# Performance work log

Measured on AMD Instinct MI355X. Metric: run time of the kernel, lower is better.

## Reference

```python
import jax, jax.numpy as jnp
import numpy as np

SCALING = 32.0 / 8.0  # alpha / rank

def setup_inputs() -> dict:
    key = jax.random.key(0)
    k1, k2, k3, k4, k5 = jax.random.split(key, 5)
    B, S, D_in, D_out, R = 4, 2048, 1600, 4800, 8
    x = jax.random.normal(k1, (B, S, D_in), dtype=jnp.float32)
    W = jax.random.normal(k2, (D_in, D_out), dtype=jnp.float32) * 0.02
    b = jax.random.normal(k3, (D_out,), dtype=jnp.float32) * 0.02
    lora_A = jax.random.normal(k4, (D_in, R), dtype=jnp.float32) * 0.02
    lora_B = jax.random.normal(k5, (R, D_out), dtype=jnp.float32) * 0.02
    return {"x": x, "W": W, "b": b, "lora_A": lora_A, "lora_B": lora_B}

def reference(x, W, b, lora_A, lora_B):
    # base Conv1D: x @ W + b  (GPT-2 Conv1D semantics)
    base = jnp.einsum('bsd,df->bsf', x, W) + b
    # low-rank LoRA path: (x @ A) @ B, scaled
    lora = jnp.einsum('bsr,rf->bsf', jnp.einsum('bsd,dr->bsr', x, lora_A), lora_B)
    return base + lora * SCALING
```

## Files before the change

### kernel.cpp

```cpp
#include <hip/hip_runtime.h>
#include <hip/hip_bf16.h>


#define M_ROWS 8192
#define K_DIM  1600
#define N_DIM  4800
#define KP     1664

#define BM 128
#define BN 160
#define BK 64
#define KT (KP / BK)

typedef __attribute__((ext_vector_type(4))) float f32x4;
typedef __attribute__((ext_vector_type(8))) short s16x8;

static __device__ __forceinline__ unsigned short f2bf(float f) {
    unsigned int u = __float_as_uint(f);
    u += 0x7fffu + ((u >> 16) & 1u);
    return (unsigned short)(u >> 16);
}

typedef __attribute__((address_space(3))) unsigned int as3_uint;
typedef __attribute__((address_space(1))) const unsigned int as1_uint;

static __device__ __forceinline__ void gl16(const unsigned short* g,
                                            unsigned short* l) {
    __builtin_amdgcn_global_load_lds((as1_uint*)g, (as3_uint*)l, 16, 0, 0);
}

__global__ __launch_bounds__(256) void prep_x(const float* __restrict__ x,
                                              const float* __restrict__ lora_A,
                                              unsigned short* __restrict__ Xbp) {
    __shared__ float4 lA4[3200];
    const int t = threadIdx.x;
    for (int g = t; g < 3200; g += 256) lA4[g] = ((const float4*)lora_A)[g];
    __syncthreads();

    const int lane = t & 63;
    const int w    = t >> 6;

    for (int i = 0; i < 4; ++i) {
        const int m = blockIdx.x * 16 + w * 4 + i;
        const float* xrow = x + (size_t)m * K_DIM;
        unsigned short* orow = Xbp + (size_t)m * KP;

        float acc[8];
#pragma unroll
        for (int r = 0; r < 8; ++r) acc[r] = 0.f;

        for (int g = lane; g < 400; g += 64) {
            float4 xv = ((const float4*)xrow)[g];
            ushort4 o;
            o.x = f2bf(xv.x); o.y = f2bf(xv.y); o.z = f2bf(xv.z); o.w = f2bf(xv.w);
            ((ushort4*)orow)[g] = o;
            float xs[4] = {xv.x, xv.y, xv.z, xv.w};
#pragma unroll
            for (int j = 0; j < 4; ++j) {
                float4 l0 = lA4[(4 * g + j) * 2 + 0];
                float4 l1 = lA4[(4 * g + j) * 2 + 1];
                acc[0] += xs[j] * l0.x; acc[1] += xs[j] * l0.y;
                acc[2] += xs[j] * l0.z; acc[3] += xs[j] * l0.w;
                acc[4] += xs[j] * l1.x; acc[5] += xs[j] * l1.y;
                acc[6] += xs[j] * l1.z; acc[7] += xs[j] * l1.w;
            }
        }

#pragma unroll
        for (int off = 32; off > 0; off >>= 1)
#pragma unroll
            for (int r = 0; r < 8; ++r) acc[r] += __shfl_down(acc[r], off, 64);

        float xa[8];
#pragma unroll
        for (int r = 0; r < 8; ++r) xa[r] = __shfl(acc[r], 0, 64);

        if (lane < 16) {
            ushort4 o;
            if (lane == 0)      { o.x = f2bf(xa[0]); o.y = f2bf(xa[1]); o.z = f2bf(xa[2]); o.w = f2bf(xa[3]); }
            else if (lane == 1) { o.x = f2bf(xa[4]); o.y = f2bf(xa[5]); o.z = f2bf(xa[6]); o.w = f2bf(xa[7]); }
            else                { o.x = 0; o.y = 0; o.z = 0; o.w = 0; }
            ((ushort4*)orow)[400 + lane] = o;
        }
    }
}

__global__ __launch_bounds__(256) void prep_w(const float* __restrict__ W,
                                              unsigned short* __restrict__ Wtp) {
    __shared__ float tile[32][65];
    const int n0 = blockIdx.x * 64;
    const int k0 = blockIdx.y * 32;
    const int t  = threadIdx.x;

#pragma unroll
    for (int p = 0; p < 2; ++p) {
        const int k  = p * 16 + (t >> 4);
        const int c4 = (t & 15) * 4;
        float4 v = *(const float4*)(W + (size_t)(k0 + k) * N_DIM + n0 + c4);
        tile[k][c4 + 0] = v.x; tile[k][c4 + 1] = v.y;
        tile[k][c4 + 2] = v.z; tile[k][c4 + 3] = v.w;
    }
    __syncthreads();

    const int n   = t >> 2;
    const int seg = t & 3;
    unsigned int pk[4];
#pragma unroll
    for (int h = 0; h < 4; ++h) {
        unsigned int lo = f2bf(tile[seg * 8 + 2 * h + 0][n]);
        unsigned int hi = f2bf(tile[seg * 8 + 2 * h + 1][n]);
        pk[h] = lo | (hi << 16);
    }
    uint4 o = {pk[0], pk[1], pk[2], pk[3]};
    *(uint4*)(Wtp + (size_t)(n0 + n) * KP + k0 + seg * 8) = o;
}

__global__ __launch_bounds__(256) void prep_lb(const float* __restrict__ lora_B,
                                               unsigned short* __restrict__ Wtp) {
    const int n = blockIdx.x * 256 + threadIdx.x;
    if (n >= N_DIM) return;
    ushort4* d4 = (ushort4*)(Wtp + (size_t)n * KP + 1600);
    ushort4 o0, o1, z;
    o0.x = f2bf(4.0f * lora_B[0 * N_DIM + n]);
    o0.y = f2bf(4.0f * lora_B[1 * N_DIM + n]);
    o0.z = f2bf(4.0f * lora_B[2 * N_DIM + n]);
    o0.w = f2bf(4.0f * lora_B[3 * N_DIM + n]);
    o1.x = f2bf(4.0f * lora_B[4 * N_DIM + n]);
    o1.y = f2bf(4.0f * lora_B[5 * N_DIM + n]);
    o1.z = f2bf(4.0f * lora_B[6 * N_DIM + n]);
    o1.w = f2bf(4.0f * lora_B[7 * N_DIM + n]);
    z.x = 0; z.y = 0; z.z = 0; z.w = 0;
    d4[0] = o0;
    d4[1] = o1;
#pragma unroll
    for (int i = 2; i < 16; ++i) d4[i] = z;
}

__global__ __launch_bounds__(256, 3) void gemm_bt(const unsigned short* __restrict__ Ab,
                                                  const unsigned short* __restrict__ Bb,
                                                  const float* __restrict__ bias,
                                                  float* __restrict__ out) {
    __shared__ unsigned short lsA[BM * BK];
    __shared__ unsigned short lsB[BN * BK];

    const int t    = threadIdx.x;
    const int n0   = blockIdx.x * BN;
    const int m0   = blockIdx.y * BM;
    const int lane = t & 63;
    const int w    = t >> 6;
    const int wr   = (w >> 1) * 64;
    const int wc   = (w & 1) * 80;
    const int lr   = lane & 15;
    const int quad = lane >> 4;

    const int rS = lane >> 3;
    const int gS = ((lane & 7) ^ (rS & 7)) * 8;
    const unsigned short* srcA = Ab + (size_t)(m0 + rS) * KP + gS;
    const unsigned short* srcB = Bb + (size_t)(n0 + rS) * KP + gS;

    int rowA[4], rowB[5];
#pragma unroll
    for (int mt = 0; mt < 4; ++mt) rowA[mt] = (wr + mt * 16 + lr) * BK;
#pragma unroll
    for (int nt = 0; nt < 5; ++nt) rowB[nt] = (wc + nt * 16 + lr) * BK;
    const int lx = lr & 7;

    f32x4 acc[4][5];
#pragma unroll
    for (int mt = 0; mt < 4; ++mt)
#pragma unroll
        for (int nt = 0; nt < 5; ++nt) acc[mt][nt] = (f32x4)0.f;

    for (int kt = 0; kt < KT; ++kt) {
        const int kb = kt * BK;
        __syncthreads();
#pragma unroll
        for (int c = w; c < 16; c += 4)
            gl16(srcA + (size_t)c * 8 * KP + kb, &lsA[c * 512]);
#pragma unroll
        for (int c = w; c < 20; c += 4)
            gl16(srcB + (size_t)c * 8 * KP + kb, &lsB[c * 512]);
        __syncthreads();

#pragma unroll
        for (int ksub = 0; ksub < 2; ++ksub) {
            const int g0 = quad + ksub * 4;
            const int koff = ((g0 ^ lx)) * 8;
            s16x8 af[4], bf[5];
#pragma unroll
            for (int mt = 0; mt < 4; ++mt) af[mt] = *(const s16x8*)&lsA[rowA[mt] + koff];
#pragma unroll
            for (int nt = 0; nt < 5; ++nt) bf[nt] = *(const s16x8*)&lsB[rowB[nt] + koff];
#pragma unroll
            for (int mt = 0; mt < 4; ++mt)
#pragma unroll
                for (int nt = 0; nt < 5; ++nt)
                    acc[mt][nt] = __builtin_amdgcn_mfma_f32_16x16x32_bf16(
                        af[mt], bf[nt], acc[mt][nt], 0, 0, 0);
        }
    }

#pragma unroll
    for (int nt = 0; nt < 5; ++nt) {
        const int gc = n0 + wc + nt * 16 + lr;
        const float bv = bias[gc];
#pragma unroll
        for (int mt = 0; mt < 4; ++mt) {
#pragma unroll
            for (int r = 0; r < 4; ++r) {
                const int grow = m0 + wr + mt * 16 + quad * 4 + r;
                out[(size_t)grow * N_DIM + gc] = acc[mt][nt][r] + bv;
            }
        }
    }
}

extern "C" void kernel_launch(void* const* d_in, const int* in_sizes, int n_in,
                              void* d_out, int out_size, void* d_ws, size_t ws_size,
                              hipStream_t stream) {
    const float* x      = (const float*)d_in[0];
    const float* W      = (const float*)d_in[1];
    const float* b      = (const float*)d_in[2];
    const float* lora_A = (const float*)d_in[3];
    const float* lora_B = (const float*)d_in[4];
    float* out = (float*)d_out;

    unsigned short* Xbp = (unsigned short*)d_ws;
    unsigned short* Wtp = Xbp + (size_t)M_ROWS * KP;

    prep_x<<<M_ROWS / 16, 256, 0, stream>>>(x, lora_A, Xbp);
    prep_w<<<dim3(N_DIM / 64, K_DIM / 32), 256, 0, stream>>>(W, Wtp);
    prep_lb<<<(N_DIM + 255) / 256, 256, 0, stream>>>(lora_B, Wtp);
    gemm_bt<<<dim3(N_DIM / BN, M_ROWS / BM), 256, 0, stream>>>(Xbp, Wtp, b, out);
}
```

Measured before the change: 386.1 us.

## Merge three prep kernels into one launch and read lora_A from global

Combines the x-conversion, W transpose and lora_B packing kernels into a single prep kernel that branches on block index. This removes two launches and lets the three independent prep jobs run concurrently. The x path now does two rows per wave, uses an xor butterfly reduction, and reads lora_A straight from global/cache instead of staging 51KB in LDS, which raises occupancy but adds redundant global reads of lora_A.

```diff
diff --git a/kernel.cpp b/kernel.cpp
--- a/kernel.cpp
+++ b/kernel.cpp
@@ -12,6 +12,10 @@
 #define BK 64
 #define KT (KP / BK)
 
+#define NXB 1024
+#define NWB (75 * 50)
+#define NLB 19
+
 typedef __attribute__((ext_vector_type(4))) float f32x4;
 typedef __attribute__((ext_vector_type(8))) short s16x8;
 
@@ -29,111 +33,132 @@
     __builtin_amdgcn_global_load_lds((as1_uint*)g, (as3_uint*)l, 16, 0, 0);
 }
 
-__global__ __launch_bounds__(256) void prep_x(const float* __restrict__ x,
-                                              const float* __restrict__ lora_A,
-                                              unsigned short* __restrict__ Xbp) {
-    __shared__ float4 lA4[3200];
-    const int t = threadIdx.x;
-    for (int g = t; g < 3200; g += 256) lA4[g] = ((const float4*)lora_A)[g];
-    __syncthreads();
-
-    const int lane = t & 63;
-    const int w    = t >> 6;
-
-    for (int i = 0; i < 4; ++i) {
-        const int m = blockIdx.x * 16 + w * 4 + i;
-        const float* xrow = x + (size_t)m * K_DIM;
-        unsigned short* orow = Xbp + (size_t)m * KP;
-
-        float acc[8];
-#pragma unroll
-        for (int r = 0; r < 8; ++r) acc[r] = 0.f;
+__global__ __launch_bounds__(256) void prep_all(const float* __restrict__ x,
+                                                const float* __restrict__ W,
+                                                const float* __restrict__ lora_A,
+                                                const float* __restrict__ lora_B,
+                                                unsigned short* __restrict__ Xbp,
+                                                unsigned short* __restrict__ Wtp) {
+    __shared__ float tile[32][65];
+    const int bid = blockIdx.x;
+    const int t   = threadIdx.x;
+
+    if (bid < NXB) {
+        const int lane = t & 63;
+        const int w    = t >> 6;
+        const int m0   = bid * 8 + w * 2;
+        const float* xr0 = x + (size_t)m0 * K_DIM;
+        const float* xr1 = xr0 + K_DIM;
+        unsigned short* o0 = Xbp + (size_t)m0 * KP;
+        unsigned short* o1 = o0 + KP;
+
+        float a0[8], a1[8];
+#pragma unroll
+        for (int r = 0; r < 8; ++r) { a0[r] = 0.f; a1[r] = 0.f; }
 
         for (int g = lane; g < 400; g += 64) {
-            float4 xv = ((const float4*)xrow)[g];
-            ushort4 o;
-            o.x = f2bf(xv.x); o.y = f2bf(xv.y); o.z = f2bf(xv.z); o.w = f2bf(xv.w);
-            ((ushort4*)orow)[g] = o;
-            float xs[4] = {xv.x, xv.y, xv.z, xv.w};
+            const float4* ap = (const float4*)(lora_A + (size_t)32 * g);
+            float4 x0 = ((const float4*)xr0)[g];
+            float4 x1 = ((const float4*)xr1)[g];
+
+            ushort4 s0, s1;
+            s0.x = f2bf(x0.x); s0.y = f2bf(x0.y); s0.z = f2bf(x0.z); s0.w = f2bf(x0.w);
+            s1.x = f2bf(x1.x); s1.y = f2bf(x1.y); s1.z = f2bf(x1.z); s1.w = f2bf(x1.w);
+            ((ushort4*)o0)[g] = s0;
+            ((ushort4*)o1)[g] = s1;
+
+            float xs0[4] = {x0.x, x0.y, x0.z, x0.w};
+            float xs1[4] = {x1.x, x1.y, x1.z, x1.w};
 #pragma unroll
             for (int j = 0; j < 4; ++j) {
-                float4 l0 = lA4[(4 * g + j) * 2 + 0];
-                float4 l1 = lA4[(4 * g + j) * 2 + 1];
-                acc[0] += xs[j] * l0.x; acc[1] += xs[j] * l0.y;
-                acc[2] += xs[j] * l0.z; acc[3] += xs[j] * l0.w;
-                acc[4] += xs[j] * l1.x; acc[5] += xs[j] * l1.y;
-                acc[6] += xs[j] * l1.z; acc[7] += xs[j] * l1.w;
-            }
-        }
-
-#pragma unroll
-        for (int off = 32; off > 0; off >>= 1)
-#pragma unroll
-            for (int r = 0; r < 8; ++r) acc[r] += __shfl_down(acc[r], off, 64);
-
-        float xa[8];
-#pragma unroll
-        for (int r = 0; r < 8; ++r) xa[r] = __shfl(acc[r], 0, 64);
+                float4 lo = ap[2 * j + 0];
+                float4 hi = ap[2 * j + 1];
+                a0[0] += xs0[j] * lo.x; a0[1] += xs0[j] * lo.y;
+                a0[2] += xs0[j] * lo.z; a0[3] += xs0[j] * lo.w;
+                a0[4] += xs0[j] * hi.x; a0[5] += xs0[j] * hi.y;
+                a0[6] += xs0[j] * hi.z; a0[7] += xs0[j] * hi.w;
+                a1[0] += xs1[j] * lo.x; a1[1] += xs1[j] * lo.y;
+                a1[2] += xs1[j] * lo.z; a1[3] += xs1[j] * lo.w;
+                a1[4] += xs1[j] * hi.x; a1[5] += xs1[j] * hi.y;
+                a1[6] += xs1[j] * hi.z; a1[7] += xs1[j] * hi.w;
+            }
+        }
+
+#pragma unroll
+        for (int off = 1; off < 64; off <<= 1) {
+#pragma unroll
+            for (int r = 0; r < 8; ++r) {
+                a0[r] += __shfl_xor(a0[r], off, 64);
+                a1[r] += __shfl_xor(a1[r], off, 64);
+            }
+        }
 
         if (lane < 16) {
-            ushort4 o;
-            if (lane == 0)      { o.x = f2bf(xa[0]); o.y = f2bf(xa[1]); o.z = f2bf(xa[2]); o.w = f2bf(xa[3]); }
-            else if (lane == 1) { o.x = f2bf(xa[4]); o.y = f2bf(xa[5]); o.z = f2bf(xa[6]); o.w = f2bf(xa[7]); }
-            else                { o.x = 0; o.y = 0; o.z = 0; o.w = 0; }
-            ((ushort4*)orow)[400 + lane] = o;
-        }
-    }
-}
-
-__global__ __launch_bounds__(256) void prep_w(const float* __restrict__ W,
-                                              unsigned short* __restrict__ Wtp) {
-    __shared__ float tile[32][65];
-    const int n0 = blockIdx.x * 64;
-    const int k0 = blockIdx.y * 32;
-    const int t  = threadIdx.x;
-
-#pragma unroll
-    for (int p = 0; p < 2; ++p) {
-        const int k  = p * 16 + (t >> 4);
-        const int c4 = (t & 15) * 4;
-        float4 v = *(const float4*)(W + (size_t)(k0 + k) * N_DIM + n0 + c4);
-        tile[k][c4 + 0] = v.x; tile[k][c4 + 1] = v.y;
-        tile[k][c4 + 2] = v.z; tile[k][c4 + 3] = v.w;
-    }
-    __syncthreads();
-
-    const int n   = t >> 2;
-    const int seg = t & 3;
-    unsigned int pk[4];
-#pragma unroll
-    for (int h = 0; h < 4; ++h) {
-        unsigned int lo = f2bf(tile[seg * 8 + 2 * h + 0][n]);
-        unsigned int hi = f2bf(tile[seg * 8 + 2 * h + 1][n]);
-        pk[h] = lo | (hi << 16);
-    }
-    uint4 o = {pk[0], pk[1], pk[2], pk[3]};
-    *(uint4*)(Wtp + (size_t)(n0 + n) * KP + k0 + seg * 8) = o;
-}
-
-__global__ __launch_bounds__(256) void prep_lb(const float* __restrict__ lora_B,
-                                               unsigned short* __restrict__ Wtp) {
-    const int n = blockIdx.x * 256 + threadIdx.x;
-    if (n >= N_DIM) return;
-    ushort4* d4 = (ushort4*)(Wtp + (size_t)n * KP + 1600);
-    ushort4 o0, o1, z;
-    o0.x = f2bf(4.0f * lora_B[0 * N_DIM + n]);
-    o0.y = f2bf(4.0f * lora_B[1 * N_DIM + n]);
-    o0.z = f2bf(4.0f * lora_B[2 * N_DIM + n]);
-    o0.w = f2bf(4.0f * lora_B[3 * N_DIM + n]);
-    o1.x = f2bf(4.0f * lora_B[4 * N_DIM + n]);
-    o1.y = f2bf(4.0f * lora_B[5 * N_DIM + n]);
-    o1.z = f2bf(4.0f * lora_B[6 * N_DIM + n]);
-    o1.w = f2bf(4.0f * lora_B[7 * N_DIM + n]);
-    z.x = 0; z.y = 0; z.z = 0; z.w = 0;
-    d4[0] = o0;
-    d4[1] = o1;
-#pragma unroll
-    for (int i = 2; i < 16; ++i) d4[i] = z;
+            ushort4 t0, t1;
+            t0.x = 0; t0.y = 0; t0.z = 0; t0.w = 0;
+            t1 = t0;
+            if (lane == 0) {
+                t0.x = f2bf(a0[0]); t0.y = f2bf(a0[1]); t0.z = f2bf(a0[2]); t0.w = f2bf(a0[3]);
+                t1.x = f2bf(a1[0]); t1.y = f2bf(a1[1]); t1.z = f2bf(a1[2]); t1.w = f2bf(a1[3]);
+            } else if (lane == 1) {
+                t0.x = f2bf(a0[4]); t0.y = f2bf(a0[5]); t0.z = f2bf(a0[6]); t0.w = f2bf(a0[7]);
+                t1.x = f2bf(a1[4]); t1.y = f2bf(a1[5]); t1.z = f2bf(a1[6]); t1.w = f2bf(a1[7]);
+            }
+            ((ushort4*)o0)[400 + lane] = t0;
+            ((ushort4*)o1)[400 + lane] = t1;
+        }
+        return;
+    }
+
+    if (bid < NXB + NWB) {
+        const int wid = bid - NXB;
+        const int n0  = (wid % 75) * 64;
+        const int k0  = (wid / 75) * 32;
+
+#pragma unroll
+        for (int p = 0; p < 2; ++p) {
+            const int k  = p * 16 + (t >> 4);
+            const int c4 = (t & 15) * 4;
+            float4 v = *(const float4*)(W + (size_t)(k0 + k) * N_DIM + n0 + c4);
+            tile[k][c4 + 0] = v.x; tile[k][c4 + 1] = v.y;
+            tile[k][c4 + 2] = v.z; tile[k][c4 + 3] = v.w;
+        }
+        __syncthreads();
+
+        const int n   = t >> 2;
+        const int seg = t & 3;
+        unsigned int pk[4];
+#pragma unroll
+        for (int h = 0; h < 4; ++h) {
+            unsigned int lo = f2bf(tile[seg * 8 + 2 * h + 0][n]);
+            unsigned int hi = f2bf(tile[seg * 8 + 2 * h + 1][n]);
+            pk[h] = lo | (hi << 16);
+        }
+        uint4 o = {pk[0], pk[1], pk[2], pk[3]};
+        *(uint4*)(Wtp + (size_t)(n0 + n) * KP + k0 + seg * 8) = o;
+        return;
+    }
+
+    {
+        const int lid = bid - (NXB + NWB);
+        const int n = lid * 256 + t;
+        if (n >= N_DIM) return;
+        ushort4* d4 = (ushort4*)(Wtp + (size_t)n * KP + 1600);
+        ushort4 o0, o1, z;
+        o0.x = f2bf(4.0f * lora_B[0 * N_DIM + n]);
+        o0.y = f2bf(4.0f * lora_B[1 * N_DIM + n]);
+        o0.z = f2bf(4.0f * lora_B[2 * N_DIM + n]);
+        o0.w = f2bf(4.0f * lora_B[3 * N_DIM + n]);
+        o1.x = f2bf(4.0f * lora_B[4 * N_DIM + n]);
+        o1.y = f2bf(4.0f * lora_B[5 * N_DIM + n]);
+        o1.z = f2bf(4.0f * lora_B[6 * N_DIM + n]);
+        o1.w = f2bf(4.0f * lora_B[7 * N_DIM + n]);
+        z.x = 0; z.y = 0; z.z = 0; z.w = 0;
+        d4[0] = o0;
+        d4[1] = o1;
+#pragma unroll
+        for (int i = 2; i < 16; ++i) d4[i] = z;
+    }
 }
 
 __global__ __launch_bounds__(256, 3) void gemm_bt(const unsigned short* __restrict__ Ab,
@@ -228,8 +253,6 @@
     unsigned short* Xbp = (unsigned short*)d_ws;
     unsigned short* Wtp = Xbp + (size_t)M_ROWS * KP;
 
-    prep_x<<<M_ROWS / 16, 256, 0, stream>>>(x, lora_A, Xbp);
-    prep_w<<<dim3(N_DIM / 64, K_DIM / 32), 256, 0, stream>>>(W, Wtp);
-    prep_lb<<<(N_DIM + 255) / 256, 256, 0, stream>>>(lora_B, Wtp);
+    prep_all<<<NXB + NWB + NLB, 256, 0, stream>>>(x, W, lora_A, lora_B, Xbp, Wtp);
     gemm_bt<<<dim3(N_DIM / BN, M_ROWS / BM), 256, 0, stream>>>(Xbp, Wtp, b, out);
 }
```

Measured after the change: 383.8 us. About the same (-0.6%).
